# Kernel optimization log

Hardware: AMD Instinct MI355X
Metric: run time of the kernel (lower is better)

## Reference

```python
import jax, jax.numpy as jnp
import numpy as np

EPS = 1e-8
B, N, W, H = 64, 8192, 64, 4
CTRL = H * (W + 1 + 1 + 3 + 1)  # 280


def setup_inputs() -> dict:
    key = jax.random.key(0)
    k1, k2, k3 = jax.random.split(key, 3)
    memory = jax.random.normal(k1, (B, N, W), dtype=jnp.float32)
    controls = jax.random.normal(k2, (B, CTRL), dtype=jnp.float32)
    prev_weights = jax.random.uniform(k3, (B, H, N), dtype=jnp.float32)
    prev_weights = prev_weights / prev_weights.sum(-1, keepdims=True)
    return {"memory": memory, "controls": controls, "prev_weights": prev_weights}


def reference(memory, controls, prev_weights):
    # memory: [B, N, W]; controls: [B, H*(W+6)]; prev_weights: [B, H, N]
    b, n, w = memory.shape
    h = prev_weights.shape[1]
    # split controls per input_partition = [W, 1, 1, 3, 1] per head
    pos = 0
    keys = controls[:, pos:pos + h * w].reshape(b, h, w); pos += h * w
    betas = controls[:, pos:pos + h].reshape(b, h, 1); pos += h
    gates = controls[:, pos:pos + h].reshape(b, h, 1); pos += h
    shifts = controls[:, pos:pos + 3 * h].reshape(b, h, 3); pos += 3 * h
    gammas = controls[:, pos:pos + h].reshape(b, h, 1)

    keys = jnp.tanh(keys)
    betas = jax.nn.softplus(betas)
    gates = jax.nn.sigmoid(gates)
    shifts = jax.nn.softmax(shifts, axis=-1)
    gammas = 1.0 + jax.nn.softplus(gammas)

    # cosine-similarity content addressing: [B, H, N]
    dots = jnp.einsum('bnw,bhw->bhn', memory, keys)
    norm = (jnp.linalg.norm(keys, axis=-1)[:, :, None]
            * jnp.linalg.norm(memory, axis=-1)[:, None, :])
    scores = dots / (norm + EPS) * betas
    w_content = jax.nn.softmax(scores, axis=-1)

    # interpolate with previous weights
    w_interp = gates * w_content + (1.0 - gates) * prev_weights

    # circular convolution with 3-tap shift kernel (torch conv2d = correlation):
    # out[i] = s0*w[i-1] + s1*w[i] + s2*w[i+1] (indices mod N)
    w_shift = (shifts[..., 0:1] * jnp.roll(w_interp, 1, axis=-1)
               + shifts[..., 1:2] * w_interp
               + shifts[..., 2:3] * jnp.roll(w_interp, -1, axis=-1))

    # sharpen and renormalize
    w_sharp = w_shift ** gammas
    w_sharp = w_sharp / (w_sharp.sum(-1, keepdims=True) + EPS)

    # read: [B, H, W]
    read_data = jnp.einsum('bnw,bhn->bhw', memory, w_sharp)
    return read_data
```

## Files before the change

kernel.cpp:

```cpp
#include <hip/hip_runtime.h>
#include <math.h>

#define B_ 64
#define N_ 8192
#define W_ 64
#define H_ 4
#define CTRL_ 280
#define EPS_ 1e-8f

__device__ __forceinline__ float softplusf(float x) {
    return fmaxf(x, 0.f) + log1pf(expf(-fabsf(x)));
}

__device__ __forceinline__ float waveReduceSum(float v) {
    #pragma unroll
    for (int m = 1; m < 64; m <<= 1) v += __shfl_xor(v, m, 64);
    return v;
}

__device__ __forceinline__ float waveReduceMax(float v) {
    #pragma unroll
    for (int m = 1; m < 64; m <<= 1) v = fmaxf(v, __shfl_xor(v, m, 64));
    return v;
}

__device__ __forceinline__ float blockReduceSum256(float v, float* scr) {
    int t = threadIdx.x;
    v = waveReduceSum(v);
    if ((t & 63) == 0) scr[t >> 6] = v;
    __syncthreads();
    float r = scr[0] + scr[1] + scr[2] + scr[3];
    __syncthreads();
    return r;
}

__device__ __forceinline__ float blockReduceMax256(float v, float* scr) {
    int t = threadIdx.x;
    v = waveReduceMax(v);
    if ((t & 63) == 0) scr[t >> 6] = v;
    __syncthreads();
    float r = fmaxf(fmaxf(scr[0], scr[1]), fmaxf(scr[2], scr[3]));
    __syncthreads();
    return r;
}

__global__ __launch_bounds__(256) void k_scores(const float* __restrict__ mem,
                                                const float* __restrict__ ctrl,
                                                float* __restrict__ scores) {
    __shared__ float tile[64 * 68];
    __shared__ float keys[H_ * 68];
    __shared__ float knorm[H_];
    __shared__ float beta[H_];
    __shared__ float sstage[H_ * 65];

    const int t  = threadIdx.x;
    const int b  = blockIdx.y;
    const int n0 = blockIdx.x * 64;

    {
        int h = t >> 6, w = t & 63;
        float kv = tanhf(ctrl[b * CTRL_ + h * W_ + w]);
        keys[h * 68 + w] = kv;
        float ss = waveReduceSum(kv * kv);
        if (w == 0) knorm[h] = sqrtf(ss);
        if (t < H_) beta[t] = softplusf(ctrl[b * CTRL_ + H_ * W_ + t]);
    }

    const float4* gbase = reinterpret_cast<const float4*>(mem + ((size_t)b * N_ + n0) * W_);
    #pragma unroll
    for (int it = 0; it < 4; ++it) {
        int f = t + it * 256;
        float4 v = gbase[f];
        int row = f >> 4, col = (f & 15) << 2;
        *reinterpret_cast<float4*>(&tile[row * 68 + col]) = v;
    }
    __syncthreads();

    {
        int row = t >> 2, h = t & 3;
        float dot = 0.f, ss = 0.f;
        #pragma unroll
        for (int wg = 0; wg < 16; ++wg) {
            float4 mv = *reinterpret_cast<const float4*>(&tile[row * 68 + wg * 4]);
            float4 kv = *reinterpret_cast<const float4*>(&keys[h * 68 + wg * 4]);
            dot += mv.x * kv.x + mv.y * kv.y + mv.z * kv.z + mv.w * kv.w;
            ss  += mv.x * mv.x + mv.y * mv.y + mv.z * mv.z + mv.w * mv.w;
        }
        float sc = dot / (sqrtf(ss) * knorm[h] + EPS_) * beta[h];
        sstage[h * 65 + row] = sc;
    }
    __syncthreads();

    {
        int h = t >> 6, r = t & 63;
        scores[((size_t)(b * H_ + h)) * N_ + n0 + r] = sstage[h * 65 + r];
    }
}

__global__ __launch_bounds__(256) void k_weights(const float* __restrict__ scores,
                                                 const float* __restrict__ ctrl,
                                                 const float* __restrict__ prev,
                                                 float* __restrict__ wsharp,
                                                 float* __restrict__ Ssum) {
    __shared__ float scr[4];
    __shared__ float firsts[256];
    __shared__ float lasts[256];

    const int t  = threadIdx.x;
    const int bh = blockIdx.x;
    const int b  = bh >> 2;
    const int h  = bh & 3;

    const float4* sp = reinterpret_cast<const float4*>(scores + (size_t)bh * N_) + t * 8;
    float s[32];
    #pragma unroll
    for (int i = 0; i < 8; ++i) {
        float4 v = sp[i];
        s[i * 4 + 0] = v.x; s[i * 4 + 1] = v.y; s[i * 4 + 2] = v.z; s[i * 4 + 3] = v.w;
    }

    float mloc = -INFINITY;
    #pragma unroll
    for (int k = 0; k < 32; ++k) mloc = fmaxf(mloc, s[k]);
    float M = blockReduceMax256(mloc, scr);

    float eloc = 0.f;
    #pragma unroll
    for (int k = 0; k < 32; ++k) eloc += expf(s[k] - M);
    float L = blockReduceSum256(eloc, scr);
    float invL = 1.f / L;

    const float4* pp = reinterpret_cast<const float4*>(prev + (size_t)bh * N_) + t * 8;
    float p[32];
    #pragma unroll
    for (int i = 0; i < 8; ++i) {
        float4 v = pp[i];
        p[i * 4 + 0] = v.x; p[i * 4 + 1] = v.y; p[i * 4 + 2] = v.z; p[i * 4 + 3] = v.w;
    }

    const float* cb = ctrl + b * CTRL_;
    float g  = 1.f / (1.f + expf(-cb[260 + h]));
    float r0 = cb[264 + 3 * h], r1 = cb[265 + 3 * h], r2 = cb[266 + 3 * h];
    float rm = fmaxf(r0, fmaxf(r1, r2));
    float e0 = expf(r0 - rm), e1 = expf(r1 - rm), e2 = expf(r2 - rm);
    float ers = 1.f / (e0 + e1 + e2);
    float s0f = e0 * ers, s1f = e1 * ers, s2f = e2 * ers;
    float gamma = 1.f + softplusf(cb[276 + h]);

    float wi[32];
    #pragma unroll
    for (int k = 0; k < 32; ++k)
        wi[k] = g * (expf(s[k] - M) * invL) + (1.f - g) * p[k];

    firsts[t] = wi[0];
    lasts[t]  = wi[31];
    __syncthreads();
    float wl = lasts[(t + 255) & 255];
    float wr = firsts[(t + 1) & 255];

    float4* wout = reinterpret_cast<float4*>(wsharp + (size_t)bh * N_) + t * 8;
    float su = 0.f;
    #pragma unroll
    for (int i = 0; i < 8; ++i) {
        float us[4];
        #pragma unroll
        for (int j = 0; j < 4; ++j) {
            int k = i * 4 + j;
            float left  = (k == 0)  ? wl : wi[k - 1];
            float right = (k == 31) ? wr : wi[k + 1];
            float wsv = s0f * left + s1f * wi[k] + s2f * right;
            float uv = powf(wsv, gamma);
            us[j] = uv;
            su += uv;
        }
        float4 o; o.x = us[0]; o.y = us[1]; o.z = us[2]; o.w = us[3];
        wout[i] = o;
    }
    float S = blockReduceSum256(su, scr);
    if (t == 0) Ssum[bh] = S;
}

__global__ __launch_bounds__(256) void k_read(const float* __restrict__ mem,
                                              const float* __restrict__ wsh,
                                              const float* __restrict__ Ssum,
                                              float* __restrict__ out) {
    __shared__ float uLDS[H_ * 256];
    __shared__ float partial[16 * 64];

    const int t  = threadIdx.x;
    const int b  = blockIdx.y;
    const int cb = blockIdx.x * 256;

    {
        int h = t >> 6, i = (t & 63) << 2;
        float inv = 1.f / (Ssum[b * H_ + h] + EPS_);
        float4 v = *reinterpret_cast<const float4*>(&wsh[((size_t)(b * H_ + h)) * N_ + cb + i]);
        float4 u; u.x = v.x * inv; u.y = v.y * inv; u.z = v.z * inv; u.w = v.w * inv;
        *reinterpret_cast<float4*>(&uLDS[h * 256 + i]) = u;
    }
    __syncthreads();

    const int wv = t >> 6, l = t & 63;
    const int rb = wv * 64;
    float acc[4][4] = {};
    const float4* gb = reinterpret_cast<const float4*>(mem + ((size_t)b * N_ + cb) * W_);

    #pragma unroll 4
    for (int it = 0; it < 16; ++it) {
        int r  = rb + it * 4 + (l >> 4);
        float4 mv = gb[(size_t)r * 16 + (l & 15)];
        #pragma unroll
        for (int h = 0; h < 4; ++h) {
            float uh = uLDS[h * 256 + r];
            acc[h][0] += mv.x * uh; acc[h][1] += mv.y * uh;
            acc[h][2] += mv.z * uh; acc[h][3] += mv.w * uh;
        }
    }

    #pragma unroll
    for (int h = 0; h < 4; ++h) {
        #pragma unroll
        for (int j = 0; j < 4; ++j) {
            acc[h][j] += __shfl_xor(acc[h][j], 16, 64);
            acc[h][j] += __shfl_xor(acc[h][j], 32, 64);
        }
    }
    if (l < 16) {
        int c0 = l << 2;
        #pragma unroll
        for (int h = 0; h < 4; ++h)
            #pragma unroll
            for (int j = 0; j < 4; ++j)
                partial[(wv * 4 + h) * 64 + c0 + j] = acc[h][j];
    }
    __syncthreads();

    {
        int h = t >> 6, w = t & 63;
        float sum = partial[(0 * 4 + h) * 64 + w] + partial[(1 * 4 + h) * 64 + w]
                  + partial[(2 * 4 + h) * 64 + w] + partial[(3 * 4 + h) * 64 + w];
        atomicAdd(&out[(size_t)(b * H_ + h) * W_ + w], sum);
    }
}

extern "C" void kernel_launch(void* const* d_in, const int* in_sizes, int n_in,
                              void* d_out, int out_size, void* d_ws, size_t ws_size,
                              hipStream_t stream) {
    const float* mem  = (const float*)d_in[0];
    const float* ctrl = (const float*)d_in[1];
    const float* prev = (const float*)d_in[2];
    float* out = (float*)d_out;

    float* scores = (float*)d_ws;
    float* wsharp = scores + (size_t)B_ * H_ * N_;
    float* ssum   = wsharp + (size_t)B_ * H_ * N_;

    hipMemsetAsync(d_out, 0, sizeof(float) * B_ * H_ * W_, stream);
    k_scores<<<dim3(N_ / 64, B_), 256, 0, stream>>>(mem, ctrl, scores);
    k_weights<<<dim3(B_ * H_), 256, 0, stream>>>(scores, ctrl, prev, wsharp, ssum);
    k_read<<<dim3(N_ / 256, B_), 256, 0, stream>>>(mem, wsharp, ssum, out);
}
```

Before: 242.9 us.

## Use fixed softmax shift by beta, fold normalization into weights kernel, drop memset

The score kernel now stores exp(score - beta) directly, because cosine similarity is bounded by 1 and so beta is a valid upper bound for the max. This removes the block max reduction and the second exp pass in the weights kernel. The weights kernel also zeroes the output and writes already-normalized sharpened weights, which removes the separate memset launch and the per-block rescale in the read kernel. The risk is underflow in exp when beta is large, though cosine scores stay within [-beta, beta].

After: 239.4 us. No clear change (-1.5%).

```diff
diff --git a/kernel.cpp b/kernel.cpp
--- a/kernel.cpp
+++ b/kernel.cpp
@@ -18,12 +18,6 @@
     return v;
 }
 
-__device__ __forceinline__ float waveReduceMax(float v) {
-    #pragma unroll
-    for (int m = 1; m < 64; m <<= 1) v = fmaxf(v, __shfl_xor(v, m, 64));
-    return v;
-}
-
 __device__ __forceinline__ float blockReduceSum256(float v, float* scr) {
     int t = threadIdx.x;
     v = waveReduceSum(v);
@@ -34,19 +28,9 @@
     return r;
 }
 
-__device__ __forceinline__ float blockReduceMax256(float v, float* scr) {
-    int t = threadIdx.x;
-    v = waveReduceMax(v);
-    if ((t & 63) == 0) scr[t >> 6] = v;
-    __syncthreads();
-    float r = fmaxf(fmaxf(scr[0], scr[1]), fmaxf(scr[2], scr[3]));
-    __syncthreads();
-    return r;
-}
-
 __global__ __launch_bounds__(256) void k_scores(const float* __restrict__ mem,
                                                 const float* __restrict__ ctrl,
-                                                float* __restrict__ scores) {
+                                                float* __restrict__ expsc) {
     __shared__ float tile[64 * 68];
     __shared__ float keys[H_ * 68];
     __shared__ float knorm[H_];
@@ -86,22 +70,23 @@
             dot += mv.x * kv.x + mv.y * kv.y + mv.z * kv.z + mv.w * kv.w;
             ss  += mv.x * mv.x + mv.y * mv.y + mv.z * mv.z + mv.w * mv.w;
         }
-        float sc = dot / (sqrtf(ss) * knorm[h] + EPS_) * beta[h];
-        sstage[h * 65 + row] = sc;
+        float bh_ = beta[h];
+        float sc = dot / (sqrtf(ss) * knorm[h] + EPS_) * bh_;
+        sstage[h * 65 + row] = expf(sc - bh_);
     }
     __syncthreads();
 
     {
         int h = t >> 6, r = t & 63;
-        scores[((size_t)(b * H_ + h)) * N_ + n0 + r] = sstage[h * 65 + r];
-    }
-}
-
-__global__ __launch_bounds__(256) void k_weights(const float* __restrict__ scores,
+        expsc[((size_t)(b * H_ + h)) * N_ + n0 + r] = sstage[h * 65 + r];
+    }
+}
+
+__global__ __launch_bounds__(256) void k_weights(const float* __restrict__ expsc,
                                                  const float* __restrict__ ctrl,
                                                  const float* __restrict__ prev,
-                                                 float* __restrict__ wsharp,
-                                                 float* __restrict__ Ssum) {
+                                                 float* __restrict__ wnorm,
+                                                 float* __restrict__ out) {
     __shared__ float scr[4];
     __shared__ float firsts[256];
     __shared__ float lasts[256];
@@ -111,32 +96,22 @@
     const int b  = bh >> 2;
     const int h  = bh & 3;
 
-    const float4* sp = reinterpret_cast<const float4*>(scores + (size_t)bh * N_) + t * 8;
-    float s[32];
+    if (t < 16) {
+        float4 z = {0.f, 0.f, 0.f, 0.f};
+        reinterpret_cast<float4*>(out + (size_t)bh * 64)[t] = z;
+    }
+
+    const float4* sp = reinterpret_cast<const float4*>(expsc + (size_t)bh * N_) + t * 8;
+    float a[32];
+    float eloc = 0.f;
     #pragma unroll
     for (int i = 0; i < 8; ++i) {
         float4 v = sp[i];
-        s[i * 4 + 0] = v.x; s[i * 4 + 1] = v.y; s[i * 4 + 2] = v.z; s[i * 4 + 3] = v.w;
-    }
-
-    float mloc = -INFINITY;
-    #pragma unroll
-    for (int k = 0; k < 32; ++k) mloc = fmaxf(mloc, s[k]);
-    float M = blockReduceMax256(mloc, scr);
-
-    float eloc = 0.f;
-    #pragma unroll
-    for (int k = 0; k < 32; ++k) eloc += expf(s[k] - M);
+        a[i * 4 + 0] = v.x; a[i * 4 + 1] = v.y; a[i * 4 + 2] = v.z; a[i * 4 + 3] = v.w;
+        eloc += v.x + v.y + v.z + v.w;
+    }
     float L = blockReduceSum256(eloc, scr);
     float invL = 1.f / L;
-
-    const float4* pp = reinterpret_cast<const float4*>(prev + (size_t)bh * N_) + t * 8;
-    float p[32];
-    #pragma unroll
-    for (int i = 0; i < 8; ++i) {
-        float4 v = pp[i];
-        p[i * 4 + 0] = v.x; p[i * 4 + 1] = v.y; p[i * 4 + 2] = v.z; p[i * 4 + 3] = v.w;
-    }
 
     const float* cb = ctrl + b * CTRL_;
     float g  = 1.f / (1.f + expf(-cb[260 + h]));
@@ -147,10 +122,18 @@
     float s0f = e0 * ers, s1f = e1 * ers, s2f = e2 * ers;
     float gamma = 1.f + softplusf(cb[276 + h]);
 
+    const float4* pp = reinterpret_cast<const float4*>(prev + (size_t)bh * N_) + t * 8;
     float wi[32];
     #pragma unroll
-    for (int k = 0; k < 32; ++k)
-        wi[k] = g * (expf(s[k] - M) * invL) + (1.f - g) * p[k];
+    for (int i = 0; i < 8; ++i) {
+        float4 v = pp[i];
+        #pragma unroll
+        for (int j = 0; j < 4; ++j) {
+            int k = i * 4 + j;
+            float pv = (j == 0) ? v.x : (j == 1) ? v.y : (j == 2) ? v.z : v.w;
+            wi[k] = g * (a[k] * invL) + (1.f - g) * pv;
+        }
+    }
 
     firsts[t] = wi[0];
     lasts[t]  = wi[31];
@@ -158,31 +141,31 @@
     float wl = lasts[(t + 255) & 255];
     float wr = firsts[(t + 1) & 255];
 
-    float4* wout = reinterpret_cast<float4*>(wsharp + (size_t)bh * N_) + t * 8;
     float su = 0.f;
     #pragma unroll
+    for (int k = 0; k < 32; ++k) {
+        float left  = (k == 0)  ? wl : wi[k - 1];
+        float right = (k == 31) ? wr : wi[k + 1];
+        float wsv = s0f * left + s1f * wi[k] + s2f * right;
+        float uv = powf(wsv, gamma);
+        a[k] = uv;
+        su += uv;
+    }
+    float S = blockReduceSum256(su, scr);
+    float invS = 1.f / (S + EPS_);
+
+    float4* wout = reinterpret_cast<float4*>(wnorm + (size_t)bh * N_) + t * 8;
+    #pragma unroll
     for (int i = 0; i < 8; ++i) {
-        float us[4];
-        #pragma unroll
-        for (int j = 0; j < 4; ++j) {
-            int k = i * 4 + j;
-            float left  = (k == 0)  ? wl : wi[k - 1];
-            float right = (k == 31) ? wr : wi[k + 1];
-            float wsv = s0f * left + s1f * wi[k] + s2f * right;
-            float uv = powf(wsv, gamma);
-            us[j] = uv;
-            su += uv;
-        }
-        float4 o; o.x = us[0]; o.y = us[1]; o.z = us[2]; o.w = us[3];
+        float4 o;
+        o.x = a[i * 4 + 0] * invS; o.y = a[i * 4 + 1] * invS;
+        o.z = a[i * 4 + 2] * invS; o.w = a[i * 4 + 3] * invS;
         wout[i] = o;
     }
-    float S = blockReduceSum256(su, scr);
-    if (t == 0) Ssum[bh] = S;
 }
 
 __global__ __launch_bounds__(256) void k_read(const float* __restrict__ mem,
-                                              const float* __restrict__ wsh,
-                                              const float* __restrict__ Ssum,
+                                              const float* __restrict__ wnorm,
                                               float* __restrict__ out) {
     __shared__ float uLDS[H_ * 256];
     __shared__ float partial[16 * 64];
@@ -193,10 +176,8 @@
 
     {
         int h = t >> 6, i = (t & 63) << 2;
-        float inv = 1.f / (Ssum[b * H_ + h] + EPS_);
-        float4 v = *reinterpret_cast<const float4*>(&wsh[((size_t)(b * H_ + h)) * N_ + cb + i]);
-        float4 u; u.x = v.x * inv; u.y = v.y * inv; u.z = v.z * inv; u.w = v.w * inv;
-        *reinterpret_cast<float4*>(&uLDS[h * 256 + i]) = u;
+        float4 v = *reinterpret_cast<const float4*>(&wnorm[((size_t)(b * H_ + h)) * N_ + cb + i]);
+        *reinterpret_cast<float4*>(&uLDS[h * 256 + i]) = v;
     }
     __syncthreads();
 
@@ -251,12 +232,10 @@
     const float* prev = (const float*)d_in[2];
     float* out = (float*)d_out;
 
-    float* scores = (float*)d_ws;
-    float* wsharp = scores + (size_t)B_ * H_ * N_;
-    float* ssum   = wsharp + (size_t)B_ * H_ * N_;
-
-    hipMemsetAsync(d_out, 0, sizeof(float) * B_ * H_ * W_, stream);
-    k_scores<<<dim3(N_ / 64, B_), 256, 0, stream>>>(mem, ctrl, scores);
-    k_weights<<<dim3(B_ * H_), 256, 0, stream>>>(scores, ctrl, prev, wsharp, ssum);
-    k_read<<<dim3(N_ / 256, B_), 256, 0, stream>>>(mem, wsharp, ssum, out);
-}
+    float* expsc = (float*)d_ws;
+    float* wnorm = expsc + (size_t)B_ * H_ * N_;
+
+    k_scores <<<dim3(N_ / 64, B_), 256, 0, stream>>>(mem, ctrl, expsc);
+    k_weights<<<dim3(B_ * H_), 256, 0, stream>>>(expsc, ctrl, prev, wnorm, out);
+    k_read   <<<dim3(N_ / 256, B_), 256, 0, stream>>>(mem, wnorm, out);
+}
```
